# Kernel optimization log

Hardware: AMD Instinct MI355X
Metric: run time of the kernel (lower is better)

Reference implementation:

```python
import jax, jax.numpy as jnp
import numpy as np

D_MODEL = 1024
NUM_HEADS = 16
D_K = D_MODEL // NUM_HEADS
S, B = 2048, 2


def setup_inputs() -> dict:
    key = jax.random.key(0)
    ks = jax.random.split(key, 11)
    lim = 1.0 / np.sqrt(D_MODEL)
    def lin(kw, kb):
        W = jax.random.uniform(kw, (D_MODEL, D_MODEL), jnp.float32, -lim, lim)
        b = jax.random.uniform(kb, (D_MODEL,), jnp.float32, -lim, lim)
        return W, b
    Wq, bq = lin(ks[0], ks[1])
    Wk, bk = lin(ks[2], ks[3])
    Wv, bv = lin(ks[4], ks[5])
    Wo, bo = lin(ks[6], ks[7])
    q = jax.random.normal(ks[8], (S, B, D_MODEL), jnp.float32)
    k = jax.random.normal(ks[9], (S, B, D_MODEL), jnp.float32)
    v = jax.random.normal(ks[10], (S, B, D_MODEL), jnp.float32)
    return {"q": q, "k": k, "v": v,
            "Wq": Wq, "bq": bq, "Wk": Wk, "bk": bk,
            "Wv": Wv, "bv": bv, "Wo": Wo, "bo": bo}


def reference(q, k, v, Wq, bq, Wk, bk, Wv, bv, Wo, bo):
    s, b, _ = q.shape
    scale = np.sqrt(D_K).astype(np.float32)
    # torch Linear: x @ W.T + b
    def proj(x, W, bias):
        y = jnp.einsum('sbd,ed->sbe', x, W) + bias
        # [S,B,D] -> [B,H,S,d_k]
        return y.reshape(s, b, NUM_HEADS, D_K).transpose(1, 2, 0, 3)
    Q = proj(q, Wq, bq)
    K = proj(k, Wk, bk)
    V = proj(v, Wv, bv)
    scores = jnp.einsum('bhsd,bhtd->bhst', Q, K) / scale  # [B,H,S,S]
    attn = jax.nn.softmax(scores, axis=-1)
    ctx = jnp.einsum('bhst,bhtd->bhsd', attn, V)  # [B,H,S,d_k]
    ctx = ctx.transpose(2, 0, 1, 3).reshape(s, b, NUM_HEADS * D_K)
    return jnp.einsum('sbd,ed->sbe', ctx, Wo) + bo
```

## Files before the change

### kernel.cpp

```cpp
#include <hip/hip_runtime.h>
#include <stdint.h>

typedef __attribute__((ext_vector_type(8))) short short8;
typedef __attribute__((ext_vector_type(4))) float f32x4;
typedef __attribute__((ext_vector_type(16))) float f32x16;

#define MFMA16(a, b, c) __builtin_amdgcn_mfma_f32_16x16x32_bf16((a), (b), (c), 0, 0, 0)
#define MFMA32(a, b, c) __builtin_amdgcn_mfma_f32_32x32x16_bf16((a), (b), (c), 0, 0, 0)

__device__ inline unsigned short f2bf(float x) {
  unsigned u = __float_as_uint(x);
  u = (u + 0x7FFFu + ((u >> 16) & 1u)) >> 16;
  return (unsigned short)u;
}

__device__ inline void gload16(const unsigned short* g, unsigned short* l) {
  __builtin_amdgcn_global_load_lds(
      (const __attribute__((address_space(1))) unsigned int*)g,
      (__attribute__((address_space(3))) unsigned int*)l, 16, 0, 0);
}

__device__ inline short8 lds8(const unsigned short* base, int byteoff) {
  return *reinterpret_cast<const short8*>(reinterpret_cast<const char*>(base) + byteoff);
}

__device__ inline unsigned cvtpk(float lo, float hi) {
  unsigned r;
  asm("v_cvt_pk_bf16_f32 %0, %1, %2" : "=v"(r) : "v"(lo), "v"(hi));
  return r;
}
__device__ inline void plswap(unsigned& a, unsigned& b) {
  asm volatile("v_permlane32_swap_b32 %0, %1" : "+v"(a), "+v"(b));
}
__device__ inline float swapadd(float v) {
  float a = v, b;
  asm volatile("v_mov_b32 %1, %0\n\tv_permlane32_swap_b32 %0, %1" : "+v"(a), "=&v"(b));
  return a + b;
}

__device__ inline short8 mk8(unsigned a, unsigned b, unsigned c, unsigned d) {
  union { unsigned u[4]; short8 v; } x;
  x.u[0] = a; x.u[1] = b; x.u[2] = c; x.u[3] = d;
  return x.v;
}

__device__ inline int swz(int row, int chunk) {
  return row * 128 + (((chunk) ^ (row & 7)) << 4);
}

__global__ __launch_bounds__(256) void cvt_bf16x(const float* __restrict__ a0,
                                                 const float* __restrict__ a1,
                                                 const float* __restrict__ a2,
                                                 const float* __restrict__ a3,
                                                 unsigned short* __restrict__ d, int per) {
  int y = blockIdx.y;
  const float* s = (y == 0) ? a0 : (y == 1) ? a1 : (y == 2) ? a2 : a3;
  int i = (blockIdx.x * 256 + threadIdx.x) * 8;
  if (i >= per) return;
  float4 v0 = *reinterpret_cast<const float4*>(s + i);
  float4 v1 = *reinterpret_cast<const float4*>(s + i + 4);
  short8 o;
  o[0] = (short)f2bf(v0.x); o[1] = (short)f2bf(v0.y);
  o[2] = (short)f2bf(v0.z); o[3] = (short)f2bf(v0.w);
  o[4] = (short)f2bf(v1.x); o[5] = (short)f2bf(v1.y);
  o[6] = (short)f2bf(v1.z); o[7] = (short)f2bf(v1.w);
  *reinterpret_cast<short8*>(d + (size_t)y * per + i) = o;
}

template <int MODE>
__global__ __launch_bounds__(256) void gemm_bt(
    const unsigned short* __restrict__ Abase, const unsigned short* __restrict__ Wbase,
    const float* __restrict__ bias0, const float* __restrict__ bias1,
    const float* __restrict__ bias2, unsigned short* __restrict__ ObaseBf,
    float* __restrict__ ObaseF, int M, int N, int K) {
  const int z = blockIdx.z;
  const unsigned short* A = Abase + (size_t)z * M * K;
  const unsigned short* W = Wbase + (size_t)z * N * K;
  const float* bias = (z == 0) ? bias0 : (z == 1 ? bias1 : bias2);

  __shared__ unsigned short As[128 * 64];
  __shared__ unsigned short Bs[128 * 64];

  const int t = threadIdx.x;
  const int lane = t & 63, w = t >> 6;
  const int wm = w >> 1, wn = w & 1;
  const int m0 = blockIdx.x * 128, n0 = blockIdx.y * 128;
  const int lrow = lane & 15, lg = lane >> 4;

  f32x4 acc[4][4] = {};

  for (int kt = 0; kt < K; kt += 64) {
    __syncthreads();
#pragma unroll
    for (int p = 0; p < 4; ++p) {
      int ci = (p * 4 + w) * 64;
      int c = ci + lane;
      int row = c >> 3, cc = (c & 7) ^ (row & 7);
      gload16(&A[(size_t)(m0 + row) * K + kt + cc * 8], &As[ci * 8]);
      gload16(&W[(size_t)(n0 + row) * K + kt + cc * 8], &Bs[ci * 8]);
    }
    __syncthreads();
#pragma unroll
    for (int kc = 0; kc < 2; ++kc) {
      short8 af[4], bfr[4];
#pragma unroll
      for (int i = 0; i < 4; ++i) {
        af[i] = *reinterpret_cast<const short8*>((const char*)As + swz(wm * 64 + i * 16 + lrow, kc * 4 + lg));
        bfr[i] = *reinterpret_cast<const short8*>((const char*)Bs + swz(wn * 64 + i * 16 + lrow, kc * 4 + lg));
      }
#pragma unroll
      for (int mi = 0; mi < 4; ++mi)
#pragma unroll
        for (int ni = 0; ni < 4; ++ni) acc[mi][ni] = MFMA16(af[mi], bfr[ni], acc[mi][ni]);
    }
  }

  const int r0 = lg * 4;
  if (MODE == 0) {
    if (z < 2) {
      unsigned short* O = ObaseBf + (size_t)z * (size_t)M * N;
#pragma unroll
      for (int mi = 0; mi < 4; ++mi)
#pragma unroll
        for (int ni = 0; ni < 4; ++ni) {
          int e = n0 + wn * 64 + ni * 16 + lrow;
          float be = bias[e];
          int h = e >> 6, d = e & 63;
#pragma unroll
          for (int r = 0; r < 4; ++r) {
            int m = m0 + wm * 64 + mi * 16 + r0 + r;
            int s = m >> 1, bb = m & 1;
            O[(((size_t)(bb * 16 + h) * 2048 + s) << 6) + d] = f2bf(acc[mi][ni][r] + be);
          }
        }
    } else {
      unsigned short* O = ObaseBf + (size_t)2 * (size_t)M * N;
#pragma unroll
      for (int mi = 0; mi < 4; ++mi)
#pragma unroll
        for (int ni = 0; ni < 4; ++ni) {
          int e = n0 + wn * 64 + ni * 16 + lrow;
          float be = bias[e];
          int h = e >> 6, d = e & 63;
#pragma unroll
          for (int r = 0; r < 4; ++r) {
            int m = m0 + wm * 64 + mi * 16 + r0 + r;
            int s = m >> 1, bb = m & 1;
            O[(((size_t)(bb * 16 + h) * 64 + d) << 11) + s] = f2bf(acc[mi][ni][r] + be);
          }
        }
    }
  } else {
    float* O = ObaseF;
#pragma unroll
    for (int mi = 0; mi < 4; ++mi)
#pragma unroll
      for (int ni = 0; ni < 4; ++ni) {
        int e = n0 + wn * 64 + ni * 16 + lrow;
        float be = bias[e];
#pragma unroll
        for (int r = 0; r < 4; ++r) {
          int m = m0 + wm * 64 + mi * 16 + r0 + r;
          O[(size_t)m * N + e] = acc[mi][ni][r] + be;
        }
      }
  }
}

__global__ __launch_bounds__(256) void attn(const unsigned short* __restrict__ Q,
                                            const unsigned short* __restrict__ K,
                                            const unsigned short* __restrict__ Vt,
                                            unsigned short* __restrict__ ctx) {
  __shared__ unsigned short Ks[2 * 4096];
  __shared__ unsigned short Vs[2 * 4096];

  const int t = threadIdx.x, lane = t & 63, wv = t >> 6;
  const int bh = blockIdx.y;
  const int q0 = blockIdx.x * 128 + wv * 32;
  const int q = lane & 31, hi = lane >> 5;
  const int fq = (q ^ (q >> 3)) & 7;
  const float KS = 0.18033688011112042f;
  const float SHIFT = 8.0f;

  const unsigned short* Qb = Q + ((size_t)bh * 2048 + q0) * 64;
  const unsigned short* Kb = K + (size_t)bh * 2048 * 64;
  const unsigned short* Vb = Vt + (size_t)bh * 64 * 2048;

  short8 qf[4];
#pragma unroll
  for (int m = 0; m < 4; ++m)
    qf[m] = *reinterpret_cast<const short8*>(&Qb[q * 64 + m * 16 + hi * 8]);

  int koff[2][4], voff[2][2][2];
#pragma unroll
  for (int st = 0; st < 2; ++st) {
    int f = fq ^ (st ? 4 : 0);
#pragma unroll
    for (int m = 0; m < 4; ++m)
      koff[st][m] = (st * 32 + q) * 128 + (((m * 2 + hi) ^ f) << 4);
  }
#pragma unroll
  for (int dh = 0; dh < 2; ++dh) {
    int f = fq ^ (dh ? 4 : 0);
#pragma unroll
    for (int st = 0; st < 2; ++st)
#pragma unroll
      for (int kc = 0; kc < 2; ++kc)
        voff[dh][st][kc] = (dh * 32 + q) * 128 + (((st * 4 + kc * 2 + hi) ^ f) << 4);
  }

  int c0 = wv * 64 + lane, c1 = (4 + wv) * 64 + lane;
  int sr0 = c0 >> 3, sr1 = c1 >> 3;
  int sc0c = ((c0 & 7) ^ ((sr0 ^ (sr0 >> 3)) & 7)) * 8;
  int sc1c = ((c1 & 7) ^ ((sr1 ^ (sr1 >> 3)) & 7)) * 8;
  const unsigned short* ks0 = Kb + (size_t)sr0 * 64 + sc0c;
  const unsigned short* ks1 = Kb + (size_t)sr1 * 64 + sc1c;
  const unsigned short* vp0 = Vb + (size_t)sr0 * 2048 + sc0c;
  const unsigned short* vp1 = Vb + (size_t)sr1 * 2048 + sc1c;

  float lsum = 0.f;
  f32x16 oa0 = {}, oa1 = {};

  gload16(ks0, &Ks[wv * 512]);
  gload16(ks1, &Ks[(4 + wv) * 512]);
  gload16(vp0, &Vs[wv * 512]);
  gload16(vp1, &Vs[(4 + wv) * 512]);
  ks0 += 4096; ks1 += 4096; vp0 += 64; vp1 += 64;
  __syncthreads();

  int curoff = 0;
  for (int tile = 0; tile < 32; ++tile) {
    int nx = curoff ^ 8192;
    gload16(ks0, (unsigned short*)((char*)Ks + nx + wv * 1024));
    gload16(ks1, (unsigned short*)((char*)Ks + nx + (4 + wv) * 1024));
    gload16(vp0, (unsigned short*)((char*)Vs + nx + wv * 1024));
    gload16(vp1, (unsigned short*)((char*)Vs + nx + (4 + wv) * 1024));
    ks0 += 4096; ks1 += 4096; vp0 += 64; vp1 += 64;

    f32x16 s0 = {}, s1 = {};
#pragma unroll
    for (int m = 0; m < 4; ++m) {
      short8 k0 = lds8(Ks, curoff + koff[0][m]);
      short8 k1 = lds8(Ks, curoff + koff[1][m]);
      s0 = MFMA32(k0, qf[m], s0);
      s1 = MFMA32(k1, qf[m], s1);
    }

#pragma unroll
    for (int st = 0; st < 2; ++st) {
      const f32x16& sv = st ? s1 : s0;
      float p[16];
#pragma unroll
      for (int i = 0; i < 16; ++i) p[i] = __builtin_amdgcn_exp2f(fmaf(sv[i], KS, -SHIFT));
      float q8[8];
#pragma unroll
      for (int i = 0; i < 8; ++i) q8[i] = p[2 * i] + p[2 * i + 1];
#pragma unroll
      for (int s2 = 4; s2 > 0; s2 >>= 1)
#pragma unroll
        for (int i = 0; i < s2; ++i) q8[i] += q8[i + s2];
      lsum += q8[0];

      unsigned w0 = cvtpk(p[0], p[1]), w1 = cvtpk(p[2], p[3]);
      unsigned w2 = cvtpk(p[4], p[5]), w3 = cvtpk(p[6], p[7]);
      plswap(w0, w2); plswap(w1, w3);
      unsigned w4 = cvtpk(p[8], p[9]), w5 = cvtpk(p[10], p[11]);
      unsigned w6 = cvtpk(p[12], p[13]), w7 = cvtpk(p[14], p[15]);
      plswap(w4, w6); plswap(w5, w7);
      short8 pa0 = mk8(w0, w1, w2, w3);
      short8 pa1 = mk8(w4, w5, w6, w7);

      oa0 = MFMA32(pa0, lds8(Vs, curoff + voff[0][st][0]), oa0);
      oa1 = MFMA32(pa0, lds8(Vs, curoff + voff[1][st][0]), oa1);
      oa0 = MFMA32(pa1, lds8(Vs, curoff + voff[0][st][1]), oa0);
      oa1 = MFMA32(pa1, lds8(Vs, curoff + voff[1][st][1]), oa1);
    }

    __syncthreads();
    curoff ^= 8192;
  }

  lsum = swapadd(lsum);
  float linv = 1.0f / lsum;
  const int b = bh >> 4, h = bh & 15;
#pragma unroll
  for (int r = 0; r < 16; ++r) {
    int qr = (r & 3) + 8 * (r >> 2) + 4 * hi;
    float li = __shfl(linv, qr);
    size_t base = ((size_t)(q0 + qr) * 2 + b) * 1024 + h * 64 + q;
    ctx[base] = f2bf(oa0[r] * li);
    ctx[base + 32] = f2bf(oa1[r] * li);
  }
}

extern "C" void kernel_launch(void* const* d_in, const int* in_sizes, int n_in, void* d_out,
                              int out_size, void* d_ws, size_t ws_size, hipStream_t stream) {
  const float* q  = (const float*)d_in[0];
  const float* k  = (const float*)d_in[1];
  const float* v  = (const float*)d_in[2];
  const float* Wq = (const float*)d_in[3];
  const float* bq = (const float*)d_in[4];
  const float* Wk = (const float*)d_in[5];
  const float* bk = (const float*)d_in[6];
  const float* Wv = (const float*)d_in[7];
  const float* bv = (const float*)d_in[8];
  const float* Wo = (const float*)d_in[9];
  const float* bo = (const float*)d_in[10];

  const size_t SZ_IN = 4194304;
  const size_t SZ_W  = 1048576;
  unsigned short* ws  = (unsigned short*)d_ws;
  unsigned short* xb  = ws;
  unsigned short* Wb  = xb + 3 * SZ_IN;
  unsigned short* QKV = Wb + 4 * SZ_W;
  unsigned short* ctx = QKV + 3 * SZ_IN;

  cvt_bf16x<<<dim3(SZ_IN / 2048, 3), 256, 0, stream>>>(q, k, v, v, xb, (int)SZ_IN);
  cvt_bf16x<<<dim3(SZ_W / 2048, 4), 256, 0, stream>>>(Wq, Wk, Wv, Wo, Wb, (int)SZ_W);

  gemm_bt<0><<<dim3(32, 8, 3), 256, 0, stream>>>(xb, Wb, bq, bk, bv, QKV, nullptr, 4096, 1024,
                                                 1024);
  attn<<<dim3(16, 32), 256, 0, stream>>>(QKV, QKV + SZ_IN, QKV + 2 * SZ_IN, ctx);
  gemm_bt<1><<<dim3(32, 8, 1), 256, 0, stream>>>(ctx, Wb + 3 * SZ_W, bo, bo, bo, nullptr,
                                                 (float*)d_out, 4096, 1024, 1024);
}
```

Before: 142.8 us.

## Deepen attention K/V pipeline to four stages and compute row sums via MFMA

Replaces the double-buffered K/V LDS pipeline with a four-buffer ring. Loads are issued three tiles ahead, with one explicit vmcnt wait and a single barrier per tile instead of two __syncthreads, and s_setprio is raised around the compute section. The softmax scale is folded into the Q projection epilogue, so the exponent becomes a bare exp2 with no fma or shift. The per-row sum is now produced by an extra MFMA against a vector of ones instead of VALU adds and a lane swap. The trade-offs are double the LDS use, extra MFMA work, possible overflow risk from dropping the shift, and the loop issuing loads past the last tile.

```diff
diff --git a/kernel.cpp b/kernel.cpp
--- a/kernel.cpp
+++ b/kernel.cpp
@@ -31,11 +31,6 @@
 }
 __device__ inline void plswap(unsigned& a, unsigned& b) {
   asm volatile("v_permlane32_swap_b32 %0, %1" : "+v"(a), "+v"(b));
-}
-__device__ inline float swapadd(float v) {
-  float a = v, b;
-  asm volatile("v_mov_b32 %1, %0\n\tv_permlane32_swap_b32 %0, %1" : "+v"(a), "=&v"(b));
-  return a + b;
 }
 
 __device__ inline short8 mk8(unsigned a, unsigned b, unsigned c, unsigned d) {
@@ -117,6 +112,7 @@
 
   const int r0 = lg * 4;
   if (MODE == 0) {
+    const float scale = (z == 0) ? 0.18033688011112042f : 1.0f;
     if (z < 2) {
       unsigned short* O = ObaseBf + (size_t)z * (size_t)M * N;
 #pragma unroll
@@ -130,7 +126,7 @@
           for (int r = 0; r < 4; ++r) {
             int m = m0 + wm * 64 + mi * 16 + r0 + r;
             int s = m >> 1, bb = m & 1;
-            O[(((size_t)(bb * 16 + h) * 2048 + s) << 6) + d] = f2bf(acc[mi][ni][r] + be);
+            O[(((size_t)(bb * 16 + h) * 2048 + s) << 6) + d] = f2bf((acc[mi][ni][r] + be) * scale);
           }
         }
     } else {
@@ -171,16 +167,14 @@
                                             const unsigned short* __restrict__ K,
                                             const unsigned short* __restrict__ Vt,
                                             unsigned short* __restrict__ ctx) {
-  __shared__ unsigned short Ks[2 * 4096];
-  __shared__ unsigned short Vs[2 * 4096];
+  __shared__ unsigned short Ks[4 * 4096];
+  __shared__ unsigned short Vs[4 * 4096];
 
   const int t = threadIdx.x, lane = t & 63, wv = t >> 6;
   const int bh = blockIdx.y;
   const int q0 = blockIdx.x * 128 + wv * 32;
   const int q = lane & 31, hi = lane >> 5;
   const int fq = (q ^ (q >> 3)) & 7;
-  const float KS = 0.18033688011112042f;
-  const float SHIFT = 8.0f;
 
   const unsigned short* Qb = Q + ((size_t)bh * 2048 + q0) * 64;
   const unsigned short* Kb = K + (size_t)bh * 2048 * 64;
@@ -190,6 +184,8 @@
 #pragma unroll
   for (int m = 0; m < 4; ++m)
     qf[m] = *reinterpret_cast<const short8*>(&Qb[q * 64 + m * 16 + hi * 8]);
+
+  const short8 ones = {0x3F80, 0x3F80, 0x3F80, 0x3F80, 0x3F80, 0x3F80, 0x3F80, 0x3F80};
 
   int koff[2][4], voff[2][2][2];
 #pragma unroll
@@ -218,30 +214,42 @@
   const unsigned short* vp0 = Vb + (size_t)sr0 * 2048 + sc0c;
   const unsigned short* vp1 = Vb + (size_t)sr1 * 2048 + sc1c;
 
-  float lsum = 0.f;
-  f32x16 oa0 = {}, oa1 = {};
-
-  gload16(ks0, &Ks[wv * 512]);
-  gload16(ks1, &Ks[(4 + wv) * 512]);
-  gload16(vp0, &Vs[wv * 512]);
-  gload16(vp1, &Vs[(4 + wv) * 512]);
-  ks0 += 4096; ks1 += 4096; vp0 += 64; vp1 += 64;
-  __syncthreads();
-
-  int curoff = 0;
+  f32x16 oa0 = {}, oa1 = {}, osum = {};
+
+#pragma unroll
+  for (int pt = 0; pt < 3; ++pt) {
+    char* kb = (char*)Ks + pt * 8192;
+    char* vb2 = (char*)Vs + pt * 8192;
+    gload16(ks0, (unsigned short*)(kb + wv * 1024));
+    gload16(ks1, (unsigned short*)(kb + (4 + wv) * 1024));
+    gload16(vp0, (unsigned short*)(vb2 + wv * 1024));
+    gload16(vp1, (unsigned short*)(vb2 + (4 + wv) * 1024));
+    ks0 += 4096; ks1 += 4096; vp0 += 64; vp1 += 64;
+  }
+
   for (int tile = 0; tile < 32; ++tile) {
-    int nx = curoff ^ 8192;
-    gload16(ks0, (unsigned short*)((char*)Ks + nx + wv * 1024));
-    gload16(ks1, (unsigned short*)((char*)Ks + nx + (4 + wv) * 1024));
-    gload16(vp0, (unsigned short*)((char*)Vs + nx + wv * 1024));
-    gload16(vp1, (unsigned short*)((char*)Vs + nx + (4 + wv) * 1024));
-    ks0 += 4096; ks1 += 4096; vp0 += 64; vp1 += 64;
+    asm volatile("s_waitcnt vmcnt(8)" ::: "memory");
+    __builtin_amdgcn_s_barrier();
+    __builtin_amdgcn_sched_barrier(0);
+
+    {
+      char* kb = (char*)Ks + ((tile + 3) & 3) * 8192;
+      char* vb2 = (char*)Vs + ((tile + 3) & 3) * 8192;
+      gload16(ks0, (unsigned short*)(kb + wv * 1024));
+      gload16(ks1, (unsigned short*)(kb + (4 + wv) * 1024));
+      gload16(vp0, (unsigned short*)(vb2 + wv * 1024));
+      gload16(vp1, (unsigned short*)(vb2 + (4 + wv) * 1024));
+      ks0 += 4096; ks1 += 4096; vp0 += 64; vp1 += 64;
+    }
+
+    const int cur = (tile & 3) * 8192;
+    __builtin_amdgcn_s_setprio(1);
 
     f32x16 s0 = {}, s1 = {};
 #pragma unroll
     for (int m = 0; m < 4; ++m) {
-      short8 k0 = lds8(Ks, curoff + koff[0][m]);
-      short8 k1 = lds8(Ks, curoff + koff[1][m]);
+      short8 k0 = lds8(Ks, cur + koff[0][m]);
+      short8 k1 = lds8(Ks, cur + koff[1][m]);
       s0 = MFMA32(k0, qf[m], s0);
       s1 = MFMA32(k1, qf[m], s1);
     }
@@ -251,15 +259,7 @@
       const f32x16& sv = st ? s1 : s0;
       float p[16];
 #pragma unroll
-      for (int i = 0; i < 16; ++i) p[i] = __builtin_amdgcn_exp2f(fmaf(sv[i], KS, -SHIFT));
-      float q8[8];
-#pragma unroll
-      for (int i = 0; i < 8; ++i) q8[i] = p[2 * i] + p[2 * i + 1];
-#pragma unroll
-      for (int s2 = 4; s2 > 0; s2 >>= 1)
-#pragma unroll
-        for (int i = 0; i < s2; ++i) q8[i] += q8[i + s2];
-      lsum += q8[0];
+      for (int i = 0; i < 16; ++i) p[i] = __builtin_amdgcn_exp2f(sv[i]);
 
       unsigned w0 = cvtpk(p[0], p[1]), w1 = cvtpk(p[2], p[3]);
       unsigned w2 = cvtpk(p[4], p[5]), w3 = cvtpk(p[6], p[7]);
@@ -270,23 +270,21 @@
       short8 pa0 = mk8(w0, w1, w2, w3);
       short8 pa1 = mk8(w4, w5, w6, w7);
 
-      oa0 = MFMA32(pa0, lds8(Vs, curoff + voff[0][st][0]), oa0);
-      oa1 = MFMA32(pa0, lds8(Vs, curoff + voff[1][st][0]), oa1);
-      oa0 = MFMA32(pa1, lds8(Vs, curoff + voff[0][st][1]), oa0);
-      oa1 = MFMA32(pa1, lds8(Vs, curoff + voff[1][st][1]), oa1);
-    }
-
-    __syncthreads();
-    curoff ^= 8192;
-  }
-
-  lsum = swapadd(lsum);
-  float linv = 1.0f / lsum;
+      osum = MFMA32(pa0, ones, osum);
+      oa0 = MFMA32(pa0, lds8(Vs, cur + voff[0][st][0]), oa0);
+      oa1 = MFMA32(pa0, lds8(Vs, cur + voff[1][st][0]), oa1);
+      osum = MFMA32(pa1, ones, osum);
+      oa0 = MFMA32(pa1, lds8(Vs, cur + voff[0][st][1]), oa0);
+      oa1 = MFMA32(pa1, lds8(Vs, cur + voff[1][st][1]), oa1);
+    }
+    __builtin_amdgcn_s_setprio(0);
+  }
+
   const int b = bh >> 4, h = bh & 15;
 #pragma unroll
   for (int r = 0; r < 16; ++r) {
     int qr = (r & 3) + 8 * (r >> 2) + 4 * hi;
-    float li = __shfl(linv, qr);
+    float li = 1.0f / osum[r];
     size_t base = ((size_t)(q0 + qr) * 2 + b) * 1024 + h * 64 + q;
     ctx[base] = f2bf(oa0[r] * li);
     ctx[base + 32] = f2bf(oa1[r] * li);
```

Result: faster. 139.8 us (-2.1%).
